# Optimization experiments

Measured on AMD Instinct MI355X. Metric: run time of the kernel, lower is better.

## Reference

```python
import jax, jax.numpy as jnp
import numpy as np

N = 100000   # n_nodes
E = 600000   # n_edges
H = 128      # hidden_dim
D1 = H // 2  # GAT hidden channels


def gat_conv(h_in, src, dst, W, a_src, a_dst, b, n):
    """Single-head PyG GATConv with default add_self_loops=True, negative_slope=0.2."""
    h = h_in @ W.T                                   # [n, out]
    sl = jnp.arange(n)
    s = jnp.concatenate([src, sl])                   # self loops appended
    d = jnp.concatenate([dst, sl])
    alpha_s = (h * a_src).sum(-1)                    # [n]
    alpha_d = (h * a_dst).sum(-1)                    # [n]
    e = jax.nn.leaky_relu(alpha_s[s] + alpha_d[d], 0.2)   # [E+n]
    m = jax.ops.segment_max(e, d, num_segments=n)    # per-dst max (stable softmax)
    w = jnp.exp(e - m[d])
    z = jax.ops.segment_sum(w, d, num_segments=n)
    attn = w / z[d]                                  # segment softmax over incoming edges
    out = jax.ops.segment_sum(attn[:, None] * h[s], d, num_segments=n)
    return out + b


def setup_inputs() -> dict:
    key = jax.random.key(0)
    ks = jax.random.split(key, 14)
    sc = 0.2
    return {
        "x": jax.random.normal(ks[0], (N, 1), jnp.float32),
        "edge_index": jax.random.randint(ks[1], (2, E), 0, N, dtype=jnp.int64),
        # GAT layer 1: 1 -> 64
        "W_gat1": jax.random.normal(ks[2], (D1, 1), jnp.float32) * sc,
        "a_src1": jax.random.normal(ks[3], (D1,), jnp.float32) * sc,
        "a_dst1": jax.random.normal(ks[4], (D1,), jnp.float32) * sc,
        "b_gat1": jnp.zeros((D1,), jnp.float32),
        # GAT layer 2: 64 -> 128
        "W_gat2": jax.random.normal(ks[5], (H, D1), jnp.float32) * sc,
        "a_src2": jax.random.normal(ks[6], (H,), jnp.float32) * sc,
        "a_dst2": jax.random.normal(ks[7], (H,), jnp.float32) * sc,
        "b_gat2": jnp.zeros((H,), jnp.float32),
        # linear1: 1 -> 128, linear2: 128 -> 128
        "W_lin1": jax.random.normal(ks[8], (H, 1), jnp.float32) * sc,
        "b_lin1": jnp.zeros((H,), jnp.float32),
        "W_lin2": jax.random.normal(ks[9], (H, H), jnp.float32) * (sc / np.sqrt(H)),
        "b_lin2": jnp.zeros((H,), jnp.float32),
    }


def reference(x, edge_index, W_gat1, a_src1, a_dst1, b_gat1,
              W_gat2, a_src2, a_dst2, b_gat2,
              W_lin1, b_lin1, W_lin2, b_lin2):
    src, dst = edge_index[0], edge_index[1]
    n = x.shape[0]
    # GAT stack (2 layers, ReLU between, none after last — PyG GAT default act)
    h = gat_conv(x, src, dst, W_gat1, a_src1, a_dst1, b_gat1, n)
    h = jax.nn.relu(h)
    h = gat_conv(h, src, dst, W_gat2, a_src2, a_dst2, b_gat2, n)   # [n, 128]
    x1 = h @ W_lin2.T + b_lin2
    x2 = x @ W_lin1.T + b_lin1
    return x2 + jax.nn.relu(x1)
```

## Files before the change

kernel.cpp:

```cpp
#include <hip/hip_runtime.h>
#include <hip/hip_fp16.h>
#include <math.h>

#define LRELU(v) ((v) > 0.f ? (v) : 0.2f * (v))
#define SLOT_STRIDE 32

using short8 = __attribute__((ext_vector_type(8))) short;
using f32x4  = __attribute__((ext_vector_type(4))) float;

__device__ __forceinline__ unsigned int f2bf(float f) {
    unsigned int u = __float_as_uint(f);
    u += 0x7fffu + ((u >> 16) & 1u);
    return u >> 16;
}

#define C_VAS 4
#define C_VAD 68
#define C_BC 132
#define C_WCT 260

__global__ void k0_precompute(const float* W1, const float* as1, const float* ad1,
                              const float* W2, const float* as2, const float* ad2,
                              const float* b2, const float* Wl2, const float* bl2,
                              float* consts, unsigned short* Whc, int* cnt, int N) {
    int b = blockIdx.x, t = threadIdx.x;
    if (b < 64) {
        float acc = 0.f;
#pragma unroll 8
        for (int j = 0; j < 128; ++j) acc += Wl2[t * 128 + j] * W2[j * 64 + b];
        consts[C_WCT + b * 128 + t] = acc;
        Whc[t * 64 + b] = (unsigned short)f2bf(acc);
    } else if (b == 64) {
        if (t < 64) {
            float vs = 0.f, vd = 0.f;
            for (int c = 0; c < 128; ++c) {
                float w = W2[c * 64 + t];
                vs += as2[c] * w;
                vd += ad2[c] * w;
            }
            consts[C_VAS + t] = vs;
            consts[C_VAD + t] = vd;
        }
        float acc = bl2[t];
        for (int j = 0; j < 128; ++j) acc += Wl2[t * 128 + j] * b2[j];
        consts[C_BC + t] = acc;
        if (t < 64) {
            float p = W1[t] * as1[t], q = W1[t] * ad1[t];
#pragma unroll
            for (int m = 1; m < 64; m <<= 1) { p += __shfl_xor(p, m); q += __shfl_xor(q, m); }
            if (t == 0) { consts[0] = p; consts[1] = q; }
        }
    } else {
        int i = (b - 65) * 128 + t;
        if (i < N) cnt[i] = 0;
    }
}

__global__ void k_fill(const int* src, const int* dst, int* cnt, int* slots, int E) {
    int e = blockIdx.x * blockDim.x + threadIdx.x;
    if (e >= E) return;
    int d = dst[e];
    int pos = atomicAdd(&cnt[d], 1);
    if (pos < SLOT_STRIDE) slots[(size_t)d * SLOT_STRIDE + pos] = src[e];
}

__global__ void kL1(const float* x, const float* consts, const int* cnt, const int* slots,
                    const float* W1, const float* b1,
                    float2* pk, float* a2d, int N) {
    int lane = threadIdx.x;
    int grp = lane >> 4, c = lane & 15;
    int i = (blockIdx.x * blockDim.y + threadIdx.y) * 4 + grp;
    if (i >= N) return;
    float cs = consts[0], cd = consts[1];
    float xi = x[i];
    float w0 = __expf(LRELU(xi * (cs + cd)));
    int n = min(cnt[i], SLOT_STRIDE);
    float w = 0.f, wxl = 0.f;
    if (c < n) {
        int s = slots[(size_t)i * SLOT_STRIDE + c];
        float xs = x[s];
        float ww = __expf(LRELU(cs * xs + cd * xi));
        w = ww; wxl = ww * xs;
    }
    if (n > 16) {
        int l2 = 16 + c;
        if (l2 < n) {
            int s = slots[(size_t)i * SLOT_STRIDE + l2];
            float xs = x[s];
            float ww = __expf(LRELU(cs * xs + cd * xi));
            w += ww; wxl += ww * xs;
        }
    }
#pragma unroll
    for (int m = 1; m < 16; m <<= 1) {
        w   += __shfl_xor(w, m);
        wxl += __shfl_xor(wxl, m);
    }
    float a1 = (w0 * xi + wxl) / (w0 + w);
    float4 W4 = *(const float4*)(W1 + 4 * c);
    float4 B4 = *(const float4*)(b1 + 4 * c);
    float h0 = fmaxf(a1 * W4.x + B4.x, 0.f);
    float h1 = fmaxf(a1 * W4.y + B4.y, 0.f);
    float h2 = fmaxf(a1 * W4.z + B4.z, 0.f);
    float h3 = fmaxf(a1 * W4.w + B4.w, 0.f);
    float4 vs = *(const float4*)(consts + C_VAS + 4 * c);
    float4 vd = *(const float4*)(consts + C_VAD + 4 * c);
    float ps = h0 * vs.x + h1 * vs.y + h2 * vs.z + h3 * vs.w;
    float pd = h0 * vd.x + h1 * vd.y + h2 * vd.z + h3 * vd.w;
#pragma unroll
    for (int m = 1; m < 16; m <<= 1) {
        ps += __shfl_xor(ps, m);
        pd += __shfl_xor(pd, m);
    }
    if (c == 0) {
        pk[i] = make_float2(a1, ps);
        a2d[i] = pd;
    }
}

#define EDGE(sidx) do {                                                       \
    int _s = (sidx);                                                          \
    float2 _p = pk[_s];                                                       \
    float _w = __expf(LRELU(_p.y + adi));                                     \
    z += _w;                                                                  \
    _Pragma("unroll")                                                         \
    for (int _j = 0; _j < 8; ++_j)                                            \
        acc[_j] += _w * fmaxf(_p.x * W1f[_j] + b1f[_j], 0.f);                 \
    } while (0)

__global__ void kL2O(const float* x, const float* consts, const int* cnt, const int* slots,
                     const float2* pk, const float* a2d, const float* W1, const float* b1,
                     const unsigned short* Whc, const float* Wl1, const float* bl1,
                     float* out, int N) {
    __shared__ unsigned short svh[64 * 72];
    int lane = threadIdx.x, wy = threadIdx.y;
    int tile = blockIdx.x * 64;
    int grp = lane >> 3, c = lane & 7;

    float W1f[8], b1f[8];
#pragma unroll
    for (int j = 0; j < 8; ++j) { W1f[j] = W1[8 * c + j]; b1f[j] = b1[8 * c + j]; }

#pragma unroll
    for (int pass = 0; pass < 2; ++pass) {
        int lr = wy * 16 + pass * 8 + grp;
        int i = tile + lr;
        if (i < N) {
            float adi = a2d[i];
            float2 pki = pk[i];
            float w0 = __expf(LRELU(pki.y + adi));
            float z = w0;
            float acc[8];
#pragma unroll
            for (int j = 0; j < 8; ++j)
                acc[j] = w0 * fmaxf(pki.x * W1f[j] + b1f[j], 0.f);
            const int4* sp4 = (const int4*)(slots + (size_t)i * SLOT_STRIDE);
            int n = min(cnt[i], SLOT_STRIDE);
            for (int b4 = 0; b4 < n; b4 += 4) {
                int4 s4 = sp4[b4 >> 2];
                int m = n - b4;
                if (m > 0) EDGE(s4.x);
                if (m > 1) EDGE(s4.y);
                if (m > 2) EDGE(s4.z);
                if (m > 3) EDGE(s4.w);
            }
            float inv = 1.f / z;
            uint4 o;
            o.x = f2bf(acc[0] * inv) | (f2bf(acc[1] * inv) << 16);
            o.y = f2bf(acc[2] * inv) | (f2bf(acc[3] * inv) << 16);
            o.z = f2bf(acc[4] * inv) | (f2bf(acc[5] * inv) << 16);
            o.w = f2bf(acc[6] * inv) | (f2bf(acc[7] * inv) << 16);
            *(uint4*)(&svh[lr * 72 + 8 * c]) = o;
        }
    }
    __syncthreads();

    int r = lane & 15, kg = lane >> 4;
    int lr = wy * 16 + r;
    int lrs = (tile + lr < N) ? lr : 0;
    short8 A0 = *(const short8*)(&svh[lrs * 72 + kg * 8]);
    short8 A1 = *(const short8*)(&svh[lrs * 72 + kg * 8 + 32]);

    f32x4 acc2[8];
#pragma unroll
    for (int ct = 0; ct < 8; ++ct) {
        const unsigned short* bp = Whc + (ct * 16 + r) * 64 + kg * 8;
        short8 B0 = *(const short8*)bp;
        short8 B1 = *(const short8*)(bp + 32);
        f32x4 cacc = {0.f, 0.f, 0.f, 0.f};
        cacc = __builtin_amdgcn_mfma_f32_16x16x32_bf16(A0, B0, cacc, 0, 0, 0);
        cacc = __builtin_amdgcn_mfma_f32_16x16x32_bf16(A1, B1, cacc, 0, 0, 0);
        acc2[ct] = cacc;
    }
    float xq[4];
#pragma unroll
    for (int q = 0; q < 4; ++q) {
        int node = tile + wy * 16 + kg * 4 + q;
        xq[q] = (node < N) ? x[node] : 0.f;
    }
#pragma unroll
    for (int ct = 0; ct < 8; ++ct) {
        int col = ct * 16 + r;
        float wl = Wl1[col], bl = bl1[col], bc = consts[C_BC + col];
#pragma unroll
        for (int q = 0; q < 4; ++q) {
            int node = tile + wy * 16 + kg * 4 + q;
            if (node < N)
                out[(size_t)node * 128 + col] = xq[q] * wl + bl + fmaxf(acc2[ct][q] + bc, 0.f);
        }
    }
}

extern "C" void kernel_launch(void* const* d_in, const int* in_sizes, int n_in,
                              void* d_out, int out_size, void* d_ws, size_t ws_size,
                              hipStream_t stream) {
    const float* x   = (const float*)d_in[0];
    const int*   ei  = (const int*)d_in[1];
    const float* W1  = (const float*)d_in[2];
    const float* as1 = (const float*)d_in[3];
    const float* ad1 = (const float*)d_in[4];
    const float* b1  = (const float*)d_in[5];
    const float* W2  = (const float*)d_in[6];
    const float* as2 = (const float*)d_in[7];
    const float* ad2 = (const float*)d_in[8];
    const float* b2  = (const float*)d_in[9];
    const float* Wl1 = (const float*)d_in[10];
    const float* bl1 = (const float*)d_in[11];
    const float* Wl2 = (const float*)d_in[12];
    const float* bl2 = (const float*)d_in[13];

    int N = in_sizes[0];
    int E = in_sizes[1] / 2;
    const int* srcp = ei;
    const int* dstp = ei + E;

    float* ws = (float*)d_ws;
    float* consts = ws;
    int*   cnt    = (int*)(ws + 8704);
    int*   slots  = cnt + N;
    float2* pk    = (float2*)(slots + (size_t)SLOT_STRIDE * N);
    float* a2d    = (float*)(pk + N);
    unsigned short* Whc = (unsigned short*)(a2d + N);

    float* outp = (float*)d_out;

    dim3 b256(256);
    dim3 bw(64, 4);

    int zb = 65 + (N + 127) / 128;
    k0_precompute<<<zb, 128, 0, stream>>>(W1, as1, ad1, W2, as2, ad2, b2, Wl2, bl2,
                                          consts, Whc, cnt, N);
    k_fill<<<(E + 255) / 256, b256, 0, stream>>>(srcp, dstp, cnt, slots, E);
    kL1<<<(N + 15) / 16, bw, 0, stream>>>(x, consts, cnt, slots, W1, b1, pk, a2d, N);
    kL2O<<<(N + 63) / 64, bw, 0, stream>>>(x, consts, cnt, slots, pk, a2d, W1, b1,
                                           Whc, Wl1, bl1, outp, N);
}
```

Measured before the change: 89.78 us.

## Build adjacency with sharded LDS atomics and per-chunk sublists instead of global atomics

Edge bucketing now runs as 16 node shards by 16 edge chunks. Each block counts edges into its shard using shared-memory atomics and writes sources into a per-chunk sublist of 8 slots, with a byte count per sublist. This replaces the global atomicAdd per edge and the separate count-zeroing pass. The cost is that every block scans its whole edge chunk, so edges are read 16 times. The slot array also grows to 128 ints per node, and the consumer kernels must walk 16 sublists of variable length.

```diff
diff --git a/kernel.cpp b/kernel.cpp
--- a/kernel.cpp
+++ b/kernel.cpp
@@ -3,7 +3,10 @@
 #include <math.h>
 
 #define LRELU(v) ((v) > 0.f ? (v) : 0.2f * (v))
-#define SLOT_STRIDE 32
+#define NSH 16
+#define NCH 16
+#define CAP3 8
+#define NODE_STRIDE 128
 
 using short8 = __attribute__((ext_vector_type(8))) short;
 using f32x4  = __attribute__((ext_vector_type(4))) float;
@@ -22,7 +25,7 @@
 __global__ void k0_precompute(const float* W1, const float* as1, const float* ad1,
                               const float* W2, const float* as2, const float* ad2,
                               const float* b2, const float* Wl2, const float* bl2,
-                              float* consts, unsigned short* Whc, int* cnt, int N) {
+                              float* consts, unsigned short* Whc) {
     int b = blockIdx.x, t = threadIdx.x;
     if (b < 64) {
         float acc = 0.f;
@@ -30,7 +33,7 @@
         for (int j = 0; j < 128; ++j) acc += Wl2[t * 128 + j] * W2[j * 64 + b];
         consts[C_WCT + b * 128 + t] = acc;
         Whc[t * 64 + b] = (unsigned short)f2bf(acc);
-    } else if (b == 64) {
+    } else {
         if (t < 64) {
             float vs = 0.f, vd = 0.f;
             for (int c = 0; c < 128; ++c) {
@@ -50,22 +53,41 @@
             for (int m = 1; m < 64; m <<= 1) { p += __shfl_xor(p, m); q += __shfl_xor(q, m); }
             if (t == 0) { consts[0] = p; consts[1] = q; }
         }
-    } else {
-        int i = (b - 65) * 128 + t;
-        if (i < N) cnt[i] = 0;
-    }
-}
-
-__global__ void k_fill(const int* src, const int* dst, int* cnt, int* slots, int E) {
-    int e = blockIdx.x * blockDim.x + threadIdx.x;
-    if (e >= E) return;
-    int d = dst[e];
-    int pos = atomicAdd(&cnt[d], 1);
-    if (pos < SLOT_STRIDE) slots[(size_t)d * SLOT_STRIDE + pos] = src[e];
-}
-
-__global__ void kL1(const float* x, const float* consts, const int* cnt, const int* slots,
-                    const float* W1, const float* b1,
+    }
+}
+
+__global__ void __launch_bounds__(1024) k_fill(const int* __restrict__ src,
+                                               const int* __restrict__ dst,
+                                               unsigned char* __restrict__ cntb,
+                                               int* __restrict__ slots,
+                                               int E, int NS3, int N) {
+    __shared__ int lcnt[6272];
+    int b = blockIdx.x;
+    int shard = b & (NSH - 1), chunk = b >> 4;
+    int lo = shard * NS3;
+    int t = threadIdx.x;
+    for (int j = t; j < NS3; j += 1024) lcnt[j] = 0;
+    __syncthreads();
+    int per = (E + NCH - 1) / NCH;
+    int e0 = chunk * per;
+    int e1 = min(e0 + per, E);
+    for (int e = e0 + t; e < e1; e += 1024) {
+        int d = dst[e] - lo;
+        if ((unsigned)d < (unsigned)NS3) {
+            int p = atomicAdd(&lcnt[d], 1);
+            if (p < CAP3)
+                slots[(size_t)(lo + d) * NODE_STRIDE + chunk * CAP3 + p] = src[e];
+        }
+    }
+    __syncthreads();
+    for (int j = t; j < NS3; j += 1024) {
+        int i = lo + j;
+        if (i < N) cntb[(size_t)i * 16 + chunk] = (unsigned char)min(lcnt[j], CAP3);
+    }
+}
+
+__global__ void kL1(const float* x, const float* consts, const uint4* cntp,
+                    const int* slots, const float* W1, const float* b1,
                     float2* pk, float* a2d, int N) {
     int lane = threadIdx.x;
     int grp = lane >> 4, c = lane & 15;
@@ -74,22 +96,16 @@
     float cs = consts[0], cd = consts[1];
     float xi = x[i];
     float w0 = __expf(LRELU(xi * (cs + cd)));
-    int n = min(cnt[i], SLOT_STRIDE);
+    uint4 cw = cntp[i];
+    unsigned wv = (c >> 2) == 0 ? cw.x : (c >> 2) == 1 ? cw.y : (c >> 2) == 2 ? cw.z : cw.w;
+    int myc = (wv >> ((c & 3) * 8)) & 0xff;
+    const int* sub = slots + (size_t)i * NODE_STRIDE + c * CAP3;
     float w = 0.f, wxl = 0.f;
-    if (c < n) {
-        int s = slots[(size_t)i * SLOT_STRIDE + c];
+    for (int p = 0; p < myc; ++p) {
+        int s = sub[p];
         float xs = x[s];
         float ww = __expf(LRELU(cs * xs + cd * xi));
-        w = ww; wxl = ww * xs;
-    }
-    if (n > 16) {
-        int l2 = 16 + c;
-        if (l2 < n) {
-            int s = slots[(size_t)i * SLOT_STRIDE + l2];
-            float xs = x[s];
-            float ww = __expf(LRELU(cs * xs + cd * xi));
-            w += ww; wxl += ww * xs;
-        }
+        w += ww; wxl += ww * xs;
     }
 #pragma unroll
     for (int m = 1; m < 16; m <<= 1) {
@@ -128,14 +144,23 @@
         acc[_j] += _w * fmaxf(_p.x * W1f[_j] + b1f[_j], 0.f);                 \
     } while (0)
 
-__global__ void kL2O(const float* x, const float* consts, const int* cnt, const int* slots,
-                     const float2* pk, const float* a2d, const float* W1, const float* b1,
-                     const unsigned short* Whc, const float* Wl1, const float* bl1,
-                     float* out, int N) {
+#define SUBLIST(wv, jw) do {                                                  \
+    unsigned _w4 = (wv);                                                      \
+    _Pragma("unroll")                                                         \
+    for (int _jb = 0; _jb < 4; ++_jb) {                                       \
+        int _cj = (_w4 >> (_jb * 8)) & 0xff;                                  \
+        const int* _sub = row + ((jw) * 4 + _jb) * CAP3;                      \
+        for (int _p = 0; _p < _cj; ++_p) EDGE(_sub[_p]);                      \
+    } } while (0)
+
+__global__ void kL2O(const float* x, const float* consts, const uint4* cntp,
+                     const int* slots, const float2* pk, const float* a2d,
+                     const float* W1, const float* b1, const unsigned short* Whc,
+                     const float* Wl1, const float* bl1, float* out, int N) {
     __shared__ unsigned short svh[64 * 72];
     int lane = threadIdx.x, wy = threadIdx.y;
     int tile = blockIdx.x * 64;
-    int grp = lane >> 3, c = lane & 7;
+    int grp8 = lane >> 3, c = lane & 7;
 
     float W1f[8], b1f[8];
 #pragma unroll
@@ -143,7 +168,7 @@
 
 #pragma unroll
     for (int pass = 0; pass < 2; ++pass) {
-        int lr = wy * 16 + pass * 8 + grp;
+        int lr = wy * 16 + pass * 8 + grp8;
         int i = tile + lr;
         if (i < N) {
             float adi = a2d[i];
@@ -154,16 +179,12 @@
 #pragma unroll
             for (int j = 0; j < 8; ++j)
                 acc[j] = w0 * fmaxf(pki.x * W1f[j] + b1f[j], 0.f);
-            const int4* sp4 = (const int4*)(slots + (size_t)i * SLOT_STRIDE);
-            int n = min(cnt[i], SLOT_STRIDE);
-            for (int b4 = 0; b4 < n; b4 += 4) {
-                int4 s4 = sp4[b4 >> 2];
-                int m = n - b4;
-                if (m > 0) EDGE(s4.x);
-                if (m > 1) EDGE(s4.y);
-                if (m > 2) EDGE(s4.z);
-                if (m > 3) EDGE(s4.w);
-            }
+            uint4 cw = cntp[i];
+            const int* row = slots + (size_t)i * NODE_STRIDE;
+            SUBLIST(cw.x, 0);
+            SUBLIST(cw.y, 1);
+            SUBLIST(cw.z, 2);
+            SUBLIST(cw.w, 3);
             float inv = 1.f / z;
             uint4 o;
             o.x = f2bf(acc[0] * inv) | (f2bf(acc[1] * inv) << 16);
@@ -234,24 +255,26 @@
     const int* srcp = ei;
     const int* dstp = ei + E;
 
+    int NS3 = (N + NSH - 1) / NSH;
+
     float* ws = (float*)d_ws;
     float* consts = ws;
-    int*   cnt    = (int*)(ws + 8704);
-    int*   slots  = cnt + N;
-    float2* pk    = (float2*)(slots + (size_t)SLOT_STRIDE * N);
+    unsigned char* cntb = (unsigned char*)(ws + 8704);
+    int*   slots  = (int*)(cntb + (size_t)16 * N);
+    float2* pk    = (float2*)(slots + (size_t)NODE_STRIDE * N);
     float* a2d    = (float*)(pk + N);
-    unsigned short* Whc = (unsigned short*)(a2d + N);
+    uintptr_t wb  = ((uintptr_t)(a2d + N) + 15) & ~(uintptr_t)15;
+    unsigned short* Whc = (unsigned short*)wb;
 
     float* outp = (float*)d_out;
 
-    dim3 b256(256);
     dim3 bw(64, 4);
 
-    int zb = 65 + (N + 127) / 128;
-    k0_precompute<<<zb, 128, 0, stream>>>(W1, as1, ad1, W2, as2, ad2, b2, Wl2, bl2,
-                                          consts, Whc, cnt, N);
-    k_fill<<<(E + 255) / 256, b256, 0, stream>>>(srcp, dstp, cnt, slots, E);
-    kL1<<<(N + 15) / 16, bw, 0, stream>>>(x, consts, cnt, slots, W1, b1, pk, a2d, N);
-    kL2O<<<(N + 63) / 64, bw, 0, stream>>>(x, consts, cnt, slots, pk, a2d, W1, b1,
-                                           Whc, Wl1, bl1, outp, N);
-}
+    k0_precompute<<<65, 128, 0, stream>>>(W1, as1, ad1, W2, as2, ad2, b2, Wl2, bl2,
+                                          consts, Whc);
+    k_fill<<<NSH * NCH, 1024, 0, stream>>>(srcp, dstp, cntb, slots, E, NS3, N);
+    kL1<<<(N + 15) / 16, bw, 0, stream>>>(x, consts, (const uint4*)cntb, slots,
+                                          W1, b1, pk, a2d, N);
+    kL2O<<<(N + 63) / 64, bw, 0, stream>>>(x, consts, (const uint4*)cntb, slots, pk, a2d,
+                                           W1, b1, Whc, Wl1, bl1, outp, N);
+}
```

Measured after the change: 112.9 us. 1.26x slower.

## Replace global-atomic edge fill with sharded two-pass LDS counting sort

Applied to the files above, without the earlier changes.

Replaces the per-edge global atomicAdd bucket fill with two kernels. Nodes are split into 16 shards and edges into 16 chunks. Each block counts in-degrees for its shard and chunk with LDS atomics, and a second pass uses per-chunk prefix offsets to place sources into slots. This removes contended global atomics and makes slot order deterministic. In exchange every block rescans its edge chunk, so dst is read many times, and only 256 blocks run.

```diff
diff --git a/kernel.cpp b/kernel.cpp
--- a/kernel.cpp
+++ b/kernel.cpp
@@ -3,6 +3,8 @@
 #include <math.h>
 
 #define LRELU(v) ((v) > 0.f ? (v) : 0.2f * (v))
+#define NSH 16
+#define NCH 16
 #define SLOT_STRIDE 32
 
 using short8 = __attribute__((ext_vector_type(8))) short;
@@ -22,7 +24,7 @@
 __global__ void k0_precompute(const float* W1, const float* as1, const float* ad1,
                               const float* W2, const float* as2, const float* ad2,
                               const float* b2, const float* Wl2, const float* bl2,
-                              float* consts, unsigned short* Whc, int* cnt, int N) {
+                              float* consts, unsigned short* Whc) {
     int b = blockIdx.x, t = threadIdx.x;
     if (b < 64) {
         float acc = 0.f;
@@ -30,7 +32,7 @@
         for (int j = 0; j < 128; ++j) acc += Wl2[t * 128 + j] * W2[j * 64 + b];
         consts[C_WCT + b * 128 + t] = acc;
         Whc[t * 64 + b] = (unsigned short)f2bf(acc);
-    } else if (b == 64) {
+    } else {
         if (t < 64) {
             float vs = 0.f, vd = 0.f;
             for (int c = 0; c < 128; ++c) {
@@ -50,18 +52,72 @@
             for (int m = 1; m < 64; m <<= 1) { p += __shfl_xor(p, m); q += __shfl_xor(q, m); }
             if (t == 0) { consts[0] = p; consts[1] = q; }
         }
-    } else {
-        int i = (b - 65) * 128 + t;
-        if (i < N) cnt[i] = 0;
-    }
-}
-
-__global__ void k_fill(const int* src, const int* dst, int* cnt, int* slots, int E) {
-    int e = blockIdx.x * blockDim.x + threadIdx.x;
-    if (e >= E) return;
-    int d = dst[e];
-    int pos = atomicAdd(&cnt[d], 1);
-    if (pos < SLOT_STRIDE) slots[(size_t)d * SLOT_STRIDE + pos] = src[e];
+    }
+}
+
+__global__ void __launch_bounds__(1024) k_count(const int* __restrict__ dst,
+                                                unsigned char* __restrict__ cntb,
+                                                int E, int NS3, int N) {
+    __shared__ int lcnt[6272];
+    int b = blockIdx.x;
+    int shard = b & (NSH - 1), chunk = b >> 4;
+    int lo = shard * NS3;
+    int t = threadIdx.x;
+    for (int j = t; j < NS3; j += 1024) lcnt[j] = 0;
+    __syncthreads();
+    int per = (E + NCH - 1) / NCH;
+    int e0 = chunk * per, e1 = min(e0 + per, E);
+    for (int e = e0 + t; e < e1; e += 1024) {
+        int d = dst[e] - lo;
+        if ((unsigned)d < (unsigned)NS3) atomicAdd(&lcnt[d], 1);
+    }
+    __syncthreads();
+    for (int j = t; j < NS3; j += 1024) {
+        int i = lo + j;
+        if (i < N) cntb[(size_t)i * 16 + chunk] = (unsigned char)min(lcnt[j], 255);
+    }
+}
+
+__global__ void __launch_bounds__(1024) k_fill2(const int* __restrict__ src,
+                                                const int* __restrict__ dst,
+                                                const unsigned char* __restrict__ cntb,
+                                                int* __restrict__ cnt,
+                                                int* __restrict__ slots,
+                                                int E, int NS3, int N) {
+    __shared__ int lcnt[6272];
+    __shared__ int lbase[6272];
+    int b = blockIdx.x;
+    int shard = b & (NSH - 1), chunk = b >> 4;
+    int lo = shard * NS3;
+    int t = threadIdx.x;
+    for (int j = t; j < NS3; j += 1024) {
+        lcnt[j] = 0;
+        int i = lo + j;
+        int base = 0, tot = 0;
+        if (i < N) {
+            uint4 cw = ((const uint4*)cntb)[i];
+            unsigned wds[4] = {cw.x, cw.y, cw.z, cw.w};
+#pragma unroll
+            for (int k = 0; k < 16; ++k) {
+                int v = (wds[k >> 2] >> ((k & 3) * 8)) & 0xff;
+                if (k < chunk) base += v;
+                tot += v;
+            }
+            if (chunk == NCH - 1) cnt[i] = min(tot, SLOT_STRIDE);
+        }
+        lbase[j] = base;
+    }
+    __syncthreads();
+    int per = (E + NCH - 1) / NCH;
+    int e0 = chunk * per, e1 = min(e0 + per, E);
+    for (int e = e0 + t; e < e1; e += 1024) {
+        int d = dst[e] - lo;
+        if ((unsigned)d < (unsigned)NS3) {
+            int p = atomicAdd(&lcnt[d], 1);
+            int pos = lbase[d] + p;
+            if (pos < SLOT_STRIDE) slots[(size_t)(lo + d) * SLOT_STRIDE + pos] = src[e];
+        }
+    }
 }
 
 __global__ void kL1(const float* x, const float* consts, const int* cnt, const int* slots,
@@ -128,14 +184,14 @@
         acc[_j] += _w * fmaxf(_p.x * W1f[_j] + b1f[_j], 0.f);                 \
     } while (0)
 
-__global__ void kL2O(const float* x, const float* consts, const int* cnt, const int* slots,
-                     const float2* pk, const float* a2d, const float* W1, const float* b1,
-                     const unsigned short* Whc, const float* Wl1, const float* bl1,
-                     float* out, int N) {
+__global__ void kL2O(const float* x, const float* consts, const int* cnt,
+                     const int* slots, const float2* pk, const float* a2d,
+                     const float* W1, const float* b1, const unsigned short* Whc,
+                     const float* Wl1, const float* bl1, float* out, int N) {
     __shared__ unsigned short svh[64 * 72];
     int lane = threadIdx.x, wy = threadIdx.y;
     int tile = blockIdx.x * 64;
-    int grp = lane >> 3, c = lane & 7;
+    int grp8 = lane >> 3, c = lane & 7;
 
     float W1f[8], b1f[8];
 #pragma unroll
@@ -143,7 +199,7 @@
 
 #pragma unroll
     for (int pass = 0; pass < 2; ++pass) {
-        int lr = wy * 16 + pass * 8 + grp;
+        int lr = wy * 16 + pass * 8 + grp8;
         int i = tile + lr;
         if (i < N) {
             float adi = a2d[i];
@@ -234,24 +290,27 @@
     const int* srcp = ei;
     const int* dstp = ei + E;
 
+    int NS3 = (N + NSH - 1) / NSH;
+
     float* ws = (float*)d_ws;
     float* consts = ws;
-    int*   cnt    = (int*)(ws + 8704);
+    unsigned char* cntb = (unsigned char*)(ws + 8704);
+    int*   cnt    = (int*)(cntb + (size_t)16 * N);
     int*   slots  = cnt + N;
     float2* pk    = (float2*)(slots + (size_t)SLOT_STRIDE * N);
     float* a2d    = (float*)(pk + N);
-    unsigned short* Whc = (unsigned short*)(a2d + N);
+    uintptr_t wb  = ((uintptr_t)(a2d + N) + 15) & ~(uintptr_t)15;
+    unsigned short* Whc = (unsigned short*)wb;
 
     float* outp = (float*)d_out;
 
-    dim3 b256(256);
     dim3 bw(64, 4);
 
-    int zb = 65 + (N + 127) / 128;
-    k0_precompute<<<zb, 128, 0, stream>>>(W1, as1, ad1, W2, as2, ad2, b2, Wl2, bl2,
-                                          consts, Whc, cnt, N);
-    k_fill<<<(E + 255) / 256, b256, 0, stream>>>(srcp, dstp, cnt, slots, E);
+    k0_precompute<<<65, 128, 0, stream>>>(W1, as1, ad1, W2, as2, ad2, b2, Wl2, bl2,
+                                          consts, Whc);
+    k_count<<<NSH * NCH, 1024, 0, stream>>>(dstp, cntb, E, NS3, N);
+    k_fill2<<<NSH * NCH, 1024, 0, stream>>>(srcp, dstp, cntb, cnt, slots, E, NS3, N);
     kL1<<<(N + 15) / 16, bw, 0, stream>>>(x, consts, cnt, slots, W1, b1, pk, a2d, N);
-    kL2O<<<(N + 63) / 64, bw, 0, stream>>>(x, consts, cnt, slots, pk, a2d, W1, b1,
-                                           Whc, Wl1, bl1, outp, N);
-}
+    kL2O<<<(N + 63) / 64, bw, 0, stream>>>(x, consts, cnt, slots, pk, a2d,
+                                           W1, b1, Whc, Wl1, bl1, outp, N);
+}
```

New measurement: 102.2 us. 1.14x slower.
